# Performance work log

Hardware: AMD Instinct MI355X
Metric: run time of the kernel (lower is better)

Reference implementation:

```python
import jax, jax.numpy as jnp
import numpy as np
import math

B, N, D, KA, H = 8, 1024, 512, 16, 8
QD = D // 4
HD = D // H


def qsplit(x):
    q = x.shape[-1] // 4
    return x[..., :q], x[..., q:2*q], x[..., 2*q:3*q], x[..., 3*q:]


def hprod(p, q):
    pr, pi, pj, pk = qsplit(p)
    qr, qi, qj, qk = qsplit(q)
    return jnp.concatenate([
        pr*qr - pi*qi - pj*qj - pk*qk,
        pr*qi + pi*qr + pj*qk - pk*qj,
        pr*qj - pi*qk + pj*qr + pk*qi,
        pr*qk + pi*qj - pj*qi + pk*qr,
    ], axis=-1)


def qconj(x):
    r, i, j, k = qsplit(x)
    return jnp.concatenate([r, -i, -j, -k], axis=-1)


def qlin(x, w, b):
    # w: [4, qo, qi] -> Hamilton block matrix [4qo, 4qi]
    r, i, j, k = w[0], w[1], w[2], w[3]
    W = jnp.concatenate([
        jnp.concatenate([r, -i, -j, -k], axis=1),
        jnp.concatenate([i,  r, -k,  j], axis=1),
        jnp.concatenate([j,  k,  r, -i], axis=1),
        jnp.concatenate([k, -j,  i,  r], axis=1),
    ], axis=0)
    return x @ W.T + b


def qln(x, gamma, beta):
    # per-component LayerNorm over Q; gamma/beta: [4, Q]
    qd = x.shape[-1] // 4
    xs = x.reshape(x.shape[:-1] + (4, qd))
    m = xs.mean(-1, keepdims=True)
    v = xs.var(-1, keepdims=True)
    y = (xs - m) / jnp.sqrt(v + 1e-5) * gamma + beta
    return y.reshape(x.shape)


def setup_inputs():
    key = jax.random.key(0)
    ks = jax.random.split(key, 20)
    lim = math.sqrt(6.0 / (2 * QD))  # xavier for [QD, QD]
    def qw(k):
        return jax.random.uniform(k, (4, QD, QD), minval=-lim, maxval=lim)
    return {
        'q': jax.random.normal(ks[0], (B, N, D), dtype=jnp.float32),
        'spike': jax.random.uniform(ks[1], (B, N), dtype=jnp.float32),
        'mask': jnp.ones((B, N), dtype=jnp.float32),
        'theta_logit': jnp.float32(0.0),
        'w_prim': qw(ks[2]), 'b_prim': jnp.zeros((D,), jnp.float32),
        'anchors': jax.random.normal(ks[3], (KA, D)) * 0.5,
        'log_sigma': jnp.zeros((KA,), jnp.float32),
        'w_aggr': qw(ks[4]), 'b_aggr': jnp.zeros((D,), jnp.float32),
        'w_q': qw(ks[5]), 'b_q': jnp.zeros((D,), jnp.float32),
        'w_k': qw(ks[6]), 'b_k': jnp.zeros((D,), jnp.float32),
        'w_v': qw(ks[7]), 'b_v': jnp.zeros((D,), jnp.float32),
        'w_o': qw(ks[8]), 'b_o': jnp.zeros((D,), jnp.float32),
        'ln_gamma': jnp.ones((4, QD), jnp.float32),
        'ln_beta': jnp.zeros((4, QD), jnp.float32),
    }


def reference(q, spike, mask, theta_logit, w_prim, b_prim, anchors, log_sigma,
              w_aggr, b_aggr, w_q, b_q, w_k, b_k, w_v, b_v, w_o, b_o,
              ln_gamma, ln_beta):
    b, n, d = q.shape
    qd = d // 4
    # --- SpikeQuaternionRotation: rotate toward K-axis by theta = theta_max*spike ---
    theta_max = (jnp.pi / 2) * jax.nn.sigmoid(theta_logit)
    theta = theta_max * spike                      # [B, N]
    c = jnp.cos(theta)[..., None]
    s = jnp.sin(theta)[..., None]
    z = jnp.zeros_like(c)
    rot = jnp.concatenate([
        jnp.broadcast_to(c, (b, n, qd)),
        jnp.broadcast_to(z, (b, n, qd)),
        jnp.broadcast_to(z, (b, n, qd)),
        jnp.broadcast_to(s, (b, n, qd)),
    ], axis=-1)
    q_rot = hprod(rot, q)                          # [B, N, D]

    # --- PrimaryLayer: per-cell quaternion transform ---
    msg_p = qlin(q_rot, w_prim, b_prim)

    # --- QuaternionAnchorLayer ---
    a_conj = qconj(anchors)                        # [KA, D]
    prod = hprod(q_rot[:, None, :, :], a_conj[None, :, None, :])  # [B, KA, N, D]
    dist = jnp.sum(prod * prod, axis=-1)           # [B, KA, N]
    sigma_sq = jnp.maximum(jnp.exp(log_sigma) ** 2, 1e-6)
    incid = jnp.exp(-dist / sigma_sq[None, :, None]) * mask[:, None, :]
    denom = jnp.maximum(incid.sum(-1, keepdims=True), 1e-6)
    h = jnp.einsum('bkn,bnd->bkd', incid, q_rot) / denom  # [B, KA, D]
    h = qlin(h, w_aggr, b_aggr)

    # --- QuaternionMHA(query=q_rot, key=h, value=h), no mask ---
    Qh = qlin(q_rot, w_q, b_q).reshape(b, n, H, HD)
    Kh = qlin(h, w_k, b_k).reshape(b, KA, H, HD)
    Vh = qlin(h, w_v, b_v).reshape(b, KA, H, HD)
    scores = jnp.einsum('bqhd,bkhd->bhqk', Qh, Kh) / jnp.sqrt(jnp.float32(HD))
    attn = jax.nn.softmax(scores, axis=-1)
    out = jnp.einsum('bhqk,bkhd->bqhd', attn, Vh).reshape(b, n, d)
    msg_a = qlin(out, w_o, b_o)

    # --- residual + per-component LayerNorm ---
    return qln(q + msg_p + msg_a, ln_gamma, ln_beta)
```

## Files before the change

kernel.cpp:

```cpp
#include <hip/hip_runtime.h>
#include <hip/hip_bf16.h>

typedef __hip_bfloat16 bf16;
typedef __attribute__((ext_vector_type(8))) short bf16x8;
typedef __attribute__((ext_vector_type(4))) float f32x4;

__device__ __forceinline__ float bflo(unsigned u) { return __uint_as_float(u << 16); }
__device__ __forceinline__ float bfhi(unsigned u) { return __uint_as_float(u & 0xffff0000u); }
__device__ __forceinline__ bool probe_f32(const void* mask) {
  return *(const unsigned*)mask == 0x3F800000u;
}
__device__ __forceinline__ float ldin(const void* p, size_t i, bool f32) {
  return f32 ? ((const float*)p)[i] : (float)((const bf16*)p)[i];
}


__global__ __launch_bounds__(256) void prologue(
    const void* w0, const void* w1, const void* w2, const void* w3,
    const void* w4, const void* w5,
    const void* b0, const void* b1, const void* b2, const void* b3,
    const void* b4, const void* b5, const void* g_, const void* be,
    const void* q, const void* spike, const void* theta_logit, const void* mask,
    bf16* __restrict__ Wall, float* __restrict__ biasF,
    bf16* __restrict__ q_rot, float* __restrict__ qn) {
  bool f32 = probe_f32(mask);
  int blk = blockIdx.x, t = threadIdx.x;
  if (blk < 1536) {
    int E = blk * 1024 + t * 4;
    int g = E >> 9;
    int wi = g >> 9;
    int o = g & 511;
    int k0 = E & 511;
    const void* src = wi == 0 ? w0 : wi == 1 ? w1 : wi == 2 ? w2 : wi == 3 ? w3 : wi == 4 ? w4 : w5;
    int ro = o >> 7, a = o & 127, co = k0 >> 7;
    int comp = ro ^ co;
    float sgn = ((0x284Eu >> (ro * 4 + co)) & 1u) ? -1.0f : 1.0f;
    bf16 ov[4];
    #pragma unroll
    for (int j = 0; j < 4; ++j) {
      int b2 = (k0 & 127) + j;
      ov[j] = (bf16)(ldin(src, comp * 16384 + a * 128 + b2, f32) * sgn);
    }
    int r = g & 63, c = k0 >> 3;
    size_t off = (size_t)(g >> 6) * 65536 + (size_t)((c >> 2) * 4096 + (r >> 4) * 1024
               + ((c & 3) * 16 + (r & 15)) * 16 + (k0 & 7) * 2);
    *(uint2*)((char*)Wall + off) = *(const uint2*)ov;
  } else if (blk < 1544) {
    int b = blk - 1536;
    const void* src = b == 0 ? b0 : b == 1 ? b1 : b == 2 ? b2 : b == 3 ? b3
                    : b == 4 ? b4 : b == 5 ? b5 : b == 6 ? g_ : be;
    biasF[b * 512 + t] = ldin(src, t, f32);
    biasF[b * 512 + 256 + t] = ldin(src, 256 + t, f32);
  } else {
    int idx = blk - 1544;
    int row = idx * 8 + (t >> 5);
    int l = (t & 31) * 4;
    float tl = ldin(theta_logit, 0, f32);
    float tmax = 1.5707963267948966f / (1.0f + __expf(-tl));
    float th = tmax * ldin(spike, row, f32);
    float c = cosf(th), s = sinf(th);
    size_t base = (size_t)row * 512;
    float av[4], bv[4], cv[4], dv[4];
    if (f32) {
      const float* qp = (const float*)q + base + l;
      f32x4 va = *(const f32x4*)(qp);
      f32x4 vb = *(const f32x4*)(qp + 128);
      f32x4 vc = *(const f32x4*)(qp + 256);
      f32x4 vd = *(const f32x4*)(qp + 384);
      #pragma unroll
      for (int j = 0; j < 4; ++j) { av[j] = va[j]; bv[j] = vb[j]; cv[j] = vc[j]; dv[j] = vd[j]; }
    } else {
      const bf16* qp = (const bf16*)q + base + l;
      uint2 ua = *(const uint2*)(qp);
      uint2 ub = *(const uint2*)(qp + 128);
      uint2 uc = *(const uint2*)(qp + 256);
      uint2 ud = *(const uint2*)(qp + 384);
      av[0] = bflo(ua.x); av[1] = bfhi(ua.x); av[2] = bflo(ua.y); av[3] = bfhi(ua.y);
      bv[0] = bflo(ub.x); bv[1] = bfhi(ub.x); bv[2] = bflo(ub.y); bv[3] = bfhi(ub.y);
      cv[0] = bflo(uc.x); cv[1] = bfhi(uc.x); cv[2] = bflo(uc.y); cv[3] = bfhi(uc.y);
      dv[0] = bflo(ud.x); dv[1] = bfhi(ud.x); dv[2] = bflo(ud.y); dv[3] = bfhi(ud.y);
    }
    bf16 o0[4], o1[4], o2[4], o3[4];
    f32x4 qv;
    #pragma unroll
    for (int j = 0; j < 4; ++j) {
      float r0 = c * av[j] - s * dv[j];
      float r1 = c * bv[j] - s * cv[j];
      float r2 = c * cv[j] + s * bv[j];
      float r3 = c * dv[j] + s * av[j];
      o0[j] = (bf16)r0; o1[j] = (bf16)r1; o2[j] = (bf16)r2; o3[j] = (bf16)r3;
      qv[j] = r0 * r0 + r1 * r1 + r2 * r2 + r3 * r3;
    }
    bf16* orow = q_rot + base + l;
    *(uint2*)(orow)       = *(const uint2*)o0;
    *(uint2*)(orow + 128) = *(const uint2*)o1;
    *(uint2*)(orow + 256) = *(const uint2*)o2;
    *(uint2*)(orow + 384) = *(const uint2*)o3;
    *(f32x4*)(qn + (size_t)row * 128 + l) = qv;
  }
}

__device__ __forceinline__ void stage_B64(const bf16* __restrict__ Bw, int n0, char* Bs, int t) {
  const char* src = (const char*)Bw + (size_t)(n0 >> 6) * 65536;
  #pragma unroll
  for (int i = 0; i < 16; ++i)
    *(uint4*)(Bs + t * 16 + i * 4096) = *(const uint4*)(src + t * 16 + i * 4096);
}

__global__ __launch_bounds__(256, 2) void gemm_dist(
    const bf16* __restrict__ A, const bf16* __restrict__ Bw,
    const float* __restrict__ bias0, const float* __restrict__ bias1,
    bf16* __restrict__ MQ,
    const float* __restrict__ qn, const void* anchors, const void* lsig,
    const void* mask, float* __restrict__ h_part, float* __restrict__ pd_part) {
  __shared__ char smem[77952];
  const int t = threadIdx.x;
  if (blockIdx.x >= 128) {
    char* Bs = smem;
    const int g = blockIdx.x - 128;
    const int wave = t >> 6, lane = t & 63;
    const int quad = lane >> 4, l16 = lane & 15;
    const int m0 = (g & 31) * 256, n0 = (g >> 5) * 64;
    stage_B64(Bw, n0, Bs, t);
    __syncthreads();
    const int mbase = m0 + wave * 64;
    f32x4 acc[4][4] = {};
    bf16x8 areg[2][4], breg[2][4];
    #pragma unroll
    for (int mt = 0; mt < 4; ++mt)
      areg[0][mt] = *(const bf16x8*)(A + (size_t)(mbase + mt * 16 + l16) * 512 + quad * 8);
    #pragma unroll
    for (int nt = 0; nt < 4; ++nt)
      breg[0][nt] = *(const bf16x8*)(Bs + nt * 1024 + lane * 16);
    #pragma unroll
    for (int kk = 0; kk < 16; ++kk) {
      const int cur = kk & 1, nxt = cur ^ 1;
      if (kk < 15) {
        const int k2 = (kk + 1) * 32;
        #pragma unroll
        for (int mt = 0; mt < 4; ++mt)
          areg[nxt][mt] = *(const bf16x8*)(A + (size_t)(mbase + mt * 16 + l16) * 512 + k2 + quad * 8);
        #pragma unroll
        for (int nt = 0; nt < 4; ++nt)
          breg[nxt][nt] = *(const bf16x8*)(Bs + (kk + 1) * 4096 + nt * 1024 + lane * 16);
      }
      #pragma unroll
      for (int mt = 0; mt < 4; ++mt)
        #pragma unroll
        for (int nt = 0; nt < 4; ++nt)
          acc[mt][nt] = __builtin_amdgcn_mfma_f32_16x16x32_bf16(areg[cur][mt], breg[cur][nt],
                                                                acc[mt][nt], 0, 0, 0);
    }
    #pragma unroll
    for (int nt = 0; nt < 4; ++nt) {
      int col = n0 + nt * 16 + l16;
      float bv = col < 512 ? bias0[col] : bias1[col - 512];
      #pragma unroll
      for (int mt = 0; mt < 4; ++mt) {
        int rb = mbase + mt * 16 + quad * 4;
        #pragma unroll
        for (int r = 0; r < 4; ++r)
          MQ[(size_t)(rb + r) * 1024 + col] = (bf16)(acc[mt][nt][r] + bv);
      }
    }
  } else {
    bool f32 = probe_f32(mask);
    bf16*  qr    = (bf16*)smem;
    float* an    = (float*)(smem + 65536);
    float* sIncT = (float*)(smem + 73728);
    float* rs    = (float*)(smem + 77824);
    float* pd    = (float*)(smem + 77888);
    int bb = blockIdx.x;
    int b = bb >> 4, nc = bb & 15;
    {
      const uint4* src = (const uint4*)((const bf16*)A + ((size_t)b * 1024 + nc * 64) * 512);
      uint4* dst = (uint4*)qr;
      #pragma unroll
      for (int i = 0; i < 16; ++i) dst[t + i * 256] = src[t + i * 256];
    }
    for (int i = t; i < 2048; i += 256) {
      int k = i >> 7, l = i & 127;
      float a0 = ldin(anchors, k * 512 + l, f32);
      float a1 = ldin(anchors, k * 512 + 128 + l, f32);
      float a2 = ldin(anchors, k * 512 + 256 + l, f32);
      float a3 = ldin(anchors, k * 512 + 384 + l, f32);
      an[i] = a0 * a0 + a1 * a1 + a2 * a2 + a3 * a3;
    }
    if (t < 16) {
      float ls = ldin(lsig, t, f32);
      float ssq = __expf(ls); ssq = fmaxf(ssq * ssq, 1e-6f);
      rs[t] = -1.0f / ssq;
      pd[t] = 0.0f;
    }
    __syncthreads();
    {
      int rl = t >> 2, part = t & 3;
      int n = nc * 64 + rl;
      const float* qrow = qn + ((size_t)b * 1024 + n) * 128 + part * 32;
      f32x4 q4[8];
      #pragma unroll
      for (int i = 0; i < 8; ++i) q4[i] = *(const f32x4*)(qrow + i * 4);
      float sc[16] = {};
      #pragma unroll
      for (int i = 0; i < 8; ++i) {
        #pragma unroll
        for (int k = 0; k < 16; ++k) {
          f32x4 av = *(const f32x4*)(an + k * 128 + part * 32 + i * 4);
          sc[k] += q4[i][0] * av[0] + q4[i][1] * av[1] + q4[i][2] * av[2] + q4[i][3] * av[3];
        }
      }
      #pragma unroll
      for (int k = 0; k < 16; ++k) {
        sc[k] += __shfl_xor(sc[k], 1, 64);
        sc[k] += __shfl_xor(sc[k], 2, 64);
      }
      if (part == 0) {
        float mval = ldin(mask, b * 1024 + n, f32);
        #pragma unroll
        for (int k = 0; k < 16; ++k) {
          float inc = __expf(sc[k] * rs[k]) * mval;
          sIncT[rl * 16 + k] = inc;
          atomicAdd(&pd[k], inc);
        }
      }
    }
    __syncthreads();
    {
      float acc0[16] = {}, acc1[16] = {};
      for (int nn = 0; nn < 64; ++nn) {
        unsigned u = *(const unsigned*)(qr + nn * 512 + 2 * t);
        float v0 = bflo(u);
        float v1 = bfhi(u);
        f32x4 p0 = *(const f32x4*)(sIncT + nn * 16);
        f32x4 p1 = *(const f32x4*)(sIncT + nn * 16 + 4);
        f32x4 p2 = *(const f32x4*)(sIncT + nn * 16 + 8);
        f32x4 p3 = *(const f32x4*)(sIncT + nn * 16 + 12);
        #pragma unroll
        for (int j = 0; j < 4; ++j) {
          acc0[j]      += p0[j] * v0; acc1[j]      += p0[j] * v1;
          acc0[4 + j]  += p1[j] * v0; acc1[4 + j]  += p1[j] * v1;
          acc0[8 + j]  += p2[j] * v0; acc1[8 + j]  += p2[j] * v1;
          acc0[12 + j] += p3[j] * v0; acc1[12 + j] += p3[j] * v1;
        }
      }
      #pragma unroll
      for (int k = 0; k < 16; ++k) {
        size_t base = ((size_t)(b * 16 + k) * 16 + nc) * 512;
        float2 o2 = {acc0[k], acc1[k]};
        *(float2*)(h_part + base + 2 * t) = o2;
      }
    }
    if (t < 16) pd_part[((size_t)(b * 16 + t)) * 16 + nc] = pd[t];
  }
}

__device__ __forceinline__ float dotW4(const char* WallB, int gRow, const float* xp512, int c4lo) {
  const char* p = WallB + (size_t)(gRow >> 6) * 65536
                + (size_t)(((gRow >> 4) & 3) * 1024 + (gRow & 15) * 16);
  float acc = 0.0f;
  #pragma unroll
  for (int c4 = c4lo; c4 < c4lo + 4; ++c4) {
    #pragma unroll
    for (int cl = 0; cl < 4; ++cl) {
      uint4 u = *(const uint4*)(p + c4 * 4096 + cl * 256);
      const float* xp = xp512 + c4 * 32 + cl * 8;
      acc += xp[0] * bflo(u.x) + xp[1] * bfhi(u.x)
           + xp[2] * bflo(u.y) + xp[3] * bfhi(u.y)
           + xp[4] * bflo(u.z) + xp[5] * bfhi(u.z)
           + xp[6] * bflo(u.w) + xp[7] * bfhi(u.w);
    }
  }
  return acc;
}

__global__ __launch_bounds__(256) void aggr_k(
    const float* __restrict__ h_part, const float* __restrict__ pd_part,
    const bf16* __restrict__ Wall, const float* __restrict__ biasF,
    float* __restrict__ h_aggr) {
  __shared__ float xs[512];
  const char* WallB = (const char*)Wall;
  const float* ba = biasF + 1536;
  const int gy = blockIdx.x >> 7, row = blockIdx.x & 127;
  const int t = threadIdx.x;
  float dsum = 0.0f;
  #pragma unroll
  for (int nc = 0; nc < 16; ++nc) dsum += pd_part[row * 16 + nc];
  float dinv = 1.0f / fmaxf(dsum, 1e-6f);
  #pragma unroll
  for (int j = 0; j < 2; ++j) {
    int d = j * 256 + t;
    float hv = 0.0f;
    #pragma unroll
    for (int nc = 0; nc < 16; ++nc) hv += h_part[(size_t)row * 8192 + nc * 512 + d];
    xs[d] = hv * dinv;
  }
  __syncthreads();
  const int o = gy * 64 + (t >> 2), part = t & 3;
  float acc = dotW4(WallB, 1536 + o, xs, part * 4);
  acc += __shfl_xor(acc, 1, 64);
  acc += __shfl_xor(acc, 2, 64);
  if (part == 0) h_aggr[(size_t)row * 512 + o] = acc + ba[o];
}

__global__ __launch_bounds__(256) void kv_k(
    const float* __restrict__ h_aggr, const bf16* __restrict__ Wall,
    const float* __restrict__ biasF,
    float* __restrict__ Kh, float* __restrict__ Vh) {
  __shared__ float ys[512];
  const char* WallB = (const char*)Wall;
  const float* bk = biasF + 2048;
  const float* bv = biasF + 2560;
  const int gy = blockIdx.x >> 7, row = blockIdx.x & 127;
  const int t = threadIdx.x;
  #pragma unroll
  for (int j = 0; j < 2; ++j) {
    int d = j * 256 + t;
    ys[d] = h_aggr[(size_t)row * 512 + d];
  }
  __syncthreads();
  const int o = gy * 64 + (t >> 2), part = t & 3;
  float ak = dotW4(WallB, 2048 + o, ys, part * 4);
  float av = dotW4(WallB, 2560 + o, ys, part * 4);
  ak += __shfl_xor(ak, 1, 64);
  ak += __shfl_xor(ak, 2, 64);
  av += __shfl_xor(av, 1, 64);
  av += __shfl_xor(av, 2, 64);
  if (part == 0) {
    Kh[(size_t)row * 512 + o] = ak + bk[o];
    Vh[(size_t)row * 512 + o] = av + bv[o];
  }
}

__global__ __launch_bounds__(256, 2) void attn_tail(
    const bf16* __restrict__ MQ, const float* __restrict__ Kh_g,
    const float* __restrict__ Vh_g, const bf16* __restrict__ Wall,
    const float* __restrict__ biasF, const void* q, const void* mask, void* out) {
  __shared__ float KV[8 * 1092];
  __shared__ float P[16 * 132];
  const bool f32 = probe_f32(mask);
  const int t = threadIdx.x;
  const int rowbase = blockIdx.x * 16;
  const int b = rowbase >> 10;
  for (int i = t; i < 8192; i += 256) {
    int k = i >> 9, d = i & 511, h = d >> 6, dd = d & 63;
    KV[h * 1092 + k * 68 + dd] = Kh_g[(size_t)b * 8192 + i];
  }
  __syncthreads();
  {
    const int r = t >> 4, h = (t >> 1) & 7, hf = t & 1;
    const int grow = rowbase + r;
    const uint4* qp = (const uint4*)(MQ + (size_t)grow * 1024 + 512 + h * 64 + hf * 32);
    float qv[32];
    #pragma unroll
    for (int i = 0; i < 4; ++i) {
      uint4 u = qp[i];
      qv[i * 8 + 0] = bflo(u.x); qv[i * 8 + 1] = bfhi(u.x);
      qv[i * 8 + 2] = bflo(u.y); qv[i * 8 + 3] = bfhi(u.y);
      qv[i * 8 + 4] = bflo(u.z); qv[i * 8 + 5] = bfhi(u.z);
      qv[i * 8 + 6] = bflo(u.w); qv[i * 8 + 7] = bfhi(u.w);
    }
    float sc[16];
    #pragma unroll
    for (int k = 0; k < 16; ++k) {
      float s = 0.0f;
      #pragma unroll
      for (int d4 = 0; d4 < 8; ++d4) {
        f32x4 kv = *(const f32x4*)(KV + h * 1092 + k * 68 + hf * 32 + d4 * 4);
        s += qv[d4 * 4 + 0] * kv[0] + qv[d4 * 4 + 1] * kv[1]
           + qv[d4 * 4 + 2] * kv[2] + qv[d4 * 4 + 3] * kv[3];
      }
      sc[k] = s;
    }
    #pragma unroll
    for (int k = 0; k < 16; ++k) sc[k] += __shfl_xor(sc[k], 1, 64);
    if (hf == 0) {
      #pragma unroll
      for (int k = 0; k < 16; ++k) sc[k] *= 0.125f;
      float m = sc[0];
      #pragma unroll
      for (int k = 1; k < 16; ++k) m = fmaxf(m, sc[k]);
      float ssum = 0.0f;
      #pragma unroll
      for (int k = 0; k < 16; ++k) { sc[k] = __expf(sc[k] - m); ssum += sc[k]; }
      float inv = 1.0f / ssum;
      #pragma unroll
      for (int k = 0; k < 16; ++k) P[r * 132 + h * 16 + k] = sc[k] * inv;
    }
  }
  __syncthreads();
  for (int i = t; i < 8192; i += 256) {
    int k = i >> 9, d = i & 511, h = d >> 6, dd = d & 63;
    KV[h * 1092 + k * 68 + dd] = Vh_g[(size_t)b * 8192 + i];
  }
  __syncthreads();
  float pv[8][4];
  {
    const int r = t >> 4, dg = t & 15;
    #pragma unroll
    for (int h = 0; h < 8; ++h) {
      float a0 = 0, a1 = 0, a2 = 0, a3 = 0;
      #pragma unroll
      for (int k = 0; k < 16; ++k) {
        float p = P[r * 132 + h * 16 + k];
        f32x4 va = *(const f32x4*)(KV + h * 1092 + k * 68 + dg * 4);
        a0 += p * va[0]; a1 += p * va[1]; a2 += p * va[2]; a3 += p * va[3];
      }
      pv[h][0] = a0; pv[h][1] = a1; pv[h][2] = a2; pv[h][3] = a3;
    }
  }
  __syncthreads();
  char* A_lds = (char*)KV;
  {
    const int r = t >> 4, dg = t & 15;
    #pragma unroll
    for (int h = 0; h < 8; ++h) {
      int c0 = h * 64 + dg * 4;
      int off = (c0 >> 5) * 1024 + ((c0 >> 3) & 3) * 256 + r * 16 + (c0 & 7) * 2;
      bf16 ov[4] = {(bf16)pv[h][0], (bf16)pv[h][1], (bf16)pv[h][2], (bf16)pv[h][3]};
      *(uint2*)(A_lds + off) = *(const uint2*)ov;
    }
  }
  __syncthreads();
  const int wave = t >> 6, lane = t & 63, quad = lane >> 4, l16 = lane & 15;
  const char* WallB = (const char*)Wall;
  f32x4 acc[8] = {};
  bf16x8 breg[2][8];
  bf16x8 areg[2];
  areg[0] = *(const bf16x8*)(A_lds + quad * 256 + l16 * 16);
  #pragma unroll
  for (int nt = 0; nt < 8; ++nt) {
    size_t cb = (size_t)(16 + wave * 2 + (nt >> 2)) * 65536;
    breg[0][nt] = *(const bf16x8*)(WallB + cb + (nt & 3) * 1024 + lane * 16);
  }
  #pragma unroll
  for (int kk = 0; kk < 16; ++kk) {
    const int cur = kk & 1, nxt = cur ^ 1;
    if (kk < 15) {
      areg[nxt] = *(const bf16x8*)(A_lds + (kk + 1) * 1024 + quad * 256 + l16 * 16);
      #pragma unroll
      for (int nt = 0; nt < 8; ++nt) {
        size_t cb = (size_t)(16 + wave * 2 + (nt >> 2)) * 65536;
        breg[nxt][nt] = *(const bf16x8*)(WallB + cb + (kk + 1) * 4096 + (nt & 3) * 1024 + lane * 16);
      }
    }
    #pragma unroll
    for (int nt = 0; nt < 8; ++nt)
      acc[nt] = __builtin_amdgcn_mfma_f32_16x16x32_bf16(areg[cur], breg[cur][nt], acc[nt], 0, 0, 0);
  }
  const float* biasO = biasF + 1024;
  const float* gamF = biasF + 3072;
  float xv[8][4];
  float s[4] = {0, 0, 0, 0}, s2[4] = {0, 0, 0, 0};
  #pragma unroll
  for (int nt = 0; nt < 8; ++nt) {
    int gcol = wave * 128 + nt * 16 + l16;
    float bo = biasO[gcol];
    #pragma unroll
    for (int reg = 0; reg < 4; ++reg) {
      int grow = rowbase + quad * 4 + reg;
      float qv = ldin(q, (size_t)grow * 512 + gcol, f32);
      float mp = (float)MQ[(size_t)grow * 1024 + gcol];
      float x = qv + mp + acc[nt][reg] + bo;
      xv[nt][reg] = x;
      s[reg] += x; s2[reg] += x * x;
    }
  }
  #pragma unroll
  for (int reg = 0; reg < 4; ++reg) {
    #pragma unroll
    for (int off = 1; off <= 8; off <<= 1) {
      s[reg]  += __shfl_xor(s[reg], off, 64);
      s2[reg] += __shfl_xor(s2[reg], off, 64);
    }
  }
  #pragma unroll
  for (int reg = 0; reg < 4; ++reg) {
    float m = s[reg] * (1.0f / 128.0f);
    float rinv = rsqrtf(s2[reg] * (1.0f / 128.0f) - m * m + 1e-5f);
    int grow = rowbase + quad * 4 + reg;
    #pragma unroll
    for (int nt = 0; nt < 8; ++nt) {
      int gcol = wave * 128 + nt * 16 + l16;
      float y = (xv[nt][reg] - m) * rinv * gamF[gcol] + gamF[512 + gcol];
      if (f32) ((float*)out)[(size_t)grow * 512 + gcol] = y;
      else     ((bf16*)out)[(size_t)grow * 512 + gcol] = (bf16)y;
    }
  }
}

extern "C" void kernel_launch(void* const* d_in, const int* in_sizes, int n_in,
                              void* d_out, int out_size, void* d_ws, size_t ws_size,
                              hipStream_t stream) {
  (void)in_sizes; (void)n_in; (void)out_size; (void)ws_size;
  const void* q      = d_in[0];
  const void* spike  = d_in[1];
  const void* mask   = d_in[2];
  const void* tl     = d_in[3];
  const void* w_prim = d_in[4];
  const void* b_prim = d_in[5];
  const void* anchors= d_in[6];
  const void* lsig   = d_in[7];
  const void* w_aggr = d_in[8];
  const void* b_aggr = d_in[9];
  const void* w_q    = d_in[10];
  const void* b_q    = d_in[11];
  const void* w_k    = d_in[12];
  const void* b_k    = d_in[13];
  const void* w_v    = d_in[14];
  const void* b_v    = d_in[15];
  const void* w_o    = d_in[16];
  const void* b_o    = d_in[17];
  const void* gam    = d_in[18];
  const void* bet    = d_in[19];

  char* ws = (char*)d_ws;
  bf16*  Wall   = (bf16*)(ws + 0);
  bf16*  q_rot  = (bf16*)(ws + 3145728);
  float* qn     = (float*)(ws + 11534336);
  bf16*  MQ     = (bf16*)(ws + 15728640);
  float* h_part = (float*)(ws + 32505856);
  float* pd_part= (float*)(ws + 36700160);
  float* Kh     = (float*)(ws + 36708352);
  float* Vh     = (float*)(ws + 36970496);
  float* biasF  = (float*)(ws + 37232640);
  float* h_aggr = (float*)(ws + 37249024);

  prologue<<<2568, 256, 0, stream>>>(w_prim, w_q, w_o, w_aggr, w_k, w_v,
                                     b_prim, b_q, b_o, b_aggr, b_k, b_v, gam, bet,
                                     q, spike, tl, mask, Wall, biasF, q_rot, qn);
  gemm_dist<<<640, 256, 0, stream>>>(q_rot, Wall, biasF + 0, biasF + 512, MQ,
                                     qn, anchors, lsig, mask, h_part, pd_part);
  aggr_k<<<1024, 256, 0, stream>>>(h_part, pd_part, Wall, biasF, h_aggr);
  kv_k<<<1024, 256, 0, stream>>>(h_aggr, Wall, biasF, Kh, Vh);
  attn_tail<<<512, 256, 0, stream>>>(MQ, Kh, Vh, Wall, biasF, q, mask, d_out);
}
```

Baseline: 189.4 us.

## Build Hamilton weight tiles on the fly instead of materializing in prologue

The prologue no longer expands five of the six quaternion weight tensors into a bf16 Hamilton block matrix in workspace. Only w_o is still expanded. The GEMM stage now builds its B tile in shared memory directly from the raw weights, applying sign and component selection while staging. The aggr and kv matvecs read the raw weights with the sign applied per quaternion block. This removes most of the prologue's weight-expansion traffic and blocks, at the cost of more scattered loads and f32-to-bf16 conversion inside the GEMM and the matvecs.

```diff
diff --git a/kernel.cpp b/kernel.cpp
--- a/kernel.cpp
+++ b/kernel.cpp
@@ -15,9 +15,8 @@
 }
 
 
-__global__ __launch_bounds__(256) void prologue(
-    const void* w0, const void* w1, const void* w2, const void* w3,
-    const void* w4, const void* w5,
+__global__ __launch_bounds__(256) void rot_k(
+    const void* w_o,
     const void* b0, const void* b1, const void* b2, const void* b3,
     const void* b4, const void* b5, const void* g_, const void* be,
     const void* q, const void* spike, const void* theta_logit, const void* mask,
@@ -25,13 +24,11 @@
     bf16* __restrict__ q_rot, float* __restrict__ qn) {
   bool f32 = probe_f32(mask);
   int blk = blockIdx.x, t = threadIdx.x;
-  if (blk < 1536) {
-    int E = blk * 1024 + t * 4;
+  if (blk < 256) {
+    int E = (blk + 512) * 1024 + t * 4;
     int g = E >> 9;
-    int wi = g >> 9;
     int o = g & 511;
     int k0 = E & 511;
-    const void* src = wi == 0 ? w0 : wi == 1 ? w1 : wi == 2 ? w2 : wi == 3 ? w3 : wi == 4 ? w4 : w5;
     int ro = o >> 7, a = o & 127, co = k0 >> 7;
     int comp = ro ^ co;
     float sgn = ((0x284Eu >> (ro * 4 + co)) & 1u) ? -1.0f : 1.0f;
@@ -39,20 +36,20 @@
     #pragma unroll
     for (int j = 0; j < 4; ++j) {
       int b2 = (k0 & 127) + j;
-      ov[j] = (bf16)(ldin(src, comp * 16384 + a * 128 + b2, f32) * sgn);
+      ov[j] = (bf16)(ldin(w_o, comp * 16384 + a * 128 + b2, f32) * sgn);
     }
     int r = g & 63, c = k0 >> 3;
     size_t off = (size_t)(g >> 6) * 65536 + (size_t)((c >> 2) * 4096 + (r >> 4) * 1024
                + ((c & 3) * 16 + (r & 15)) * 16 + (k0 & 7) * 2);
     *(uint2*)((char*)Wall + off) = *(const uint2*)ov;
-  } else if (blk < 1544) {
-    int b = blk - 1536;
+  } else if (blk < 264) {
+    int b = blk - 256;
     const void* src = b == 0 ? b0 : b == 1 ? b1 : b == 2 ? b2 : b == 3 ? b3
                     : b == 4 ? b4 : b == 5 ? b5 : b == 6 ? g_ : be;
     biasF[b * 512 + t] = ldin(src, t, f32);
     biasF[b * 512 + 256 + t] = ldin(src, 256 + t, f32);
   } else {
-    int idx = blk - 1544;
+    int idx = blk - 264;
     int row = idx * 8 + (t >> 5);
     int l = (t & 31) * 4;
     float tl = ldin(theta_logit, 0, f32);
@@ -100,28 +97,54 @@
   }
 }
 
-__device__ __forceinline__ void stage_B64(const bf16* __restrict__ Bw, int n0, char* Bs, int t) {
-  const char* src = (const char*)Bw + (size_t)(n0 >> 6) * 65536;
-  #pragma unroll
-  for (int i = 0; i < 16; ++i)
-    *(uint4*)(Bs + t * 16 + i * 4096) = *(const uint4*)(src + t * 16 + i * 4096);
+__device__ __forceinline__ void stage_B64_raw(const void* w, bool f32, int o_base, char* Bs, int t) {
+  const int r = t & 63, co = t >> 6;
+  const int o = o_base + r;
+  const int ro = o >> 7, a = o & 127;
+  const int comp = ro ^ co;
+  const bool neg = (0x284Eu >> (ro * 4 + co)) & 1u;
+  if (!f32) {
+    const char* src = (const char*)w + (size_t)(comp * 16384 + a * 128) * 2;
+    const unsigned sx = neg ? 0x80008000u : 0u;
+    #pragma unroll
+    for (int i = 0; i < 16; ++i) {
+      uint4 u = *(const uint4*)(src + i * 16);
+      u.x ^= sx; u.y ^= sx; u.z ^= sx; u.w ^= sx;
+      int off = (co * 4 + (i >> 2)) * 4096 + (r >> 4) * 1024 + ((i & 3) * 16 + (r & 15)) * 16;
+      *(uint4*)(Bs + off) = u;
+    }
+  } else {
+    const float* src = (const float*)w + comp * 16384 + a * 128;
+    const float sgn = neg ? -1.0f : 1.0f;
+    #pragma unroll
+    for (int i = 0; i < 16; ++i) {
+      f32x4 v0 = *(const f32x4*)(src + i * 8);
+      f32x4 v1 = *(const f32x4*)(src + i * 8 + 4);
+      bf16 ov[8];
+      #pragma unroll
+      for (int j = 0; j < 4; ++j) { ov[j] = (bf16)(v0[j] * sgn); ov[4 + j] = (bf16)(v1[j] * sgn); }
+      int off = (co * 4 + (i >> 2)) * 4096 + (r >> 4) * 1024 + ((i & 3) * 16 + (r & 15)) * 16;
+      *(uint4*)(Bs + off) = *(const uint4*)ov;
+    }
+  }
 }
 
 __global__ __launch_bounds__(256, 2) void gemm_dist(
-    const bf16* __restrict__ A, const bf16* __restrict__ Bw,
+    const bf16* __restrict__ A, const void* w_prim, const void* w_q,
     const float* __restrict__ bias0, const float* __restrict__ bias1,
     bf16* __restrict__ MQ,
     const float* __restrict__ qn, const void* anchors, const void* lsig,
     const void* mask, float* __restrict__ h_part, float* __restrict__ pd_part) {
   __shared__ char smem[77952];
   const int t = threadIdx.x;
+  const bool f32 = probe_f32(mask);
   if (blockIdx.x >= 128) {
     char* Bs = smem;
     const int g = blockIdx.x - 128;
     const int wave = t >> 6, lane = t & 63;
     const int quad = lane >> 4, l16 = lane & 15;
     const int m0 = (g & 31) * 256, n0 = (g >> 5) * 64;
-    stage_B64(Bw, n0, Bs, t);
+    stage_B64_raw(n0 < 512 ? w_prim : w_q, f32, n0 & 511, Bs, t);
     __syncthreads();
     const int mbase = m0 + wave * 64;
     f32x4 acc[4][4] = {};
@@ -164,7 +187,6 @@
       }
     }
   } else {
-    bool f32 = probe_f32(mask);
     bf16*  qr    = (bf16*)smem;
     float* an    = (float*)(smem + 65536);
     float* sIncT = (float*)(smem + 73728);
@@ -254,31 +276,42 @@
   }
 }
 
-__device__ __forceinline__ float dotW4(const char* WallB, int gRow, const float* xp512, int c4lo) {
-  const char* p = WallB + (size_t)(gRow >> 6) * 65536
-                + (size_t)(((gRow >> 4) & 3) * 1024 + (gRow & 15) * 16);
+__device__ __forceinline__ float dotW_raw(const void* w, bool f32, int o, int co,
+                                          const float* xp512) {
+  const int ro = o >> 7, a = o & 127;
+  const int comp = ro ^ co;
+  const float sgn = ((0x284Eu >> (ro * 4 + co)) & 1u) ? -1.0f : 1.0f;
+  const float* xp = xp512 + co * 128;
   float acc = 0.0f;
-  #pragma unroll
-  for (int c4 = c4lo; c4 < c4lo + 4; ++c4) {
-    #pragma unroll
-    for (int cl = 0; cl < 4; ++cl) {
-      uint4 u = *(const uint4*)(p + c4 * 4096 + cl * 256);
-      const float* xp = xp512 + c4 * 32 + cl * 8;
-      acc += xp[0] * bflo(u.x) + xp[1] * bfhi(u.x)
-           + xp[2] * bflo(u.y) + xp[3] * bfhi(u.y)
-           + xp[4] * bflo(u.z) + xp[5] * bfhi(u.z)
-           + xp[6] * bflo(u.w) + xp[7] * bfhi(u.w);
-    }
-  }
-  return acc;
+  if (!f32) {
+    const uint4* src = (const uint4*)((const char*)w + (size_t)(comp * 16384 + a * 128) * 2);
+    #pragma unroll
+    for (int j = 0; j < 16; ++j) {
+      uint4 u = src[j];
+      const float* x8 = xp + j * 8;
+      acc += x8[0] * bflo(u.x) + x8[1] * bfhi(u.x)
+           + x8[2] * bflo(u.y) + x8[3] * bfhi(u.y)
+           + x8[4] * bflo(u.z) + x8[5] * bfhi(u.z)
+           + x8[6] * bflo(u.w) + x8[7] * bfhi(u.w);
+    }
+  } else {
+    const float* src = (const float*)w + comp * 16384 + a * 128;
+    #pragma unroll
+    for (int j = 0; j < 32; ++j) {
+      f32x4 v = *(const f32x4*)(src + j * 4);
+      const float* x4 = xp + j * 4;
+      acc += x4[0] * v[0] + x4[1] * v[1] + x4[2] * v[2] + x4[3] * v[3];
+    }
+  }
+  return acc * sgn;
 }
 
 __global__ __launch_bounds__(256) void aggr_k(
     const float* __restrict__ h_part, const float* __restrict__ pd_part,
-    const bf16* __restrict__ Wall, const float* __restrict__ biasF,
+    const void* w_aggr, const void* mask, const float* __restrict__ biasF,
     float* __restrict__ h_aggr) {
   __shared__ float xs[512];
-  const char* WallB = (const char*)Wall;
+  const bool f32 = probe_f32(mask);
   const float* ba = biasF + 1536;
   const int gy = blockIdx.x >> 7, row = blockIdx.x & 127;
   const int t = threadIdx.x;
@@ -296,18 +329,18 @@
   }
   __syncthreads();
   const int o = gy * 64 + (t >> 2), part = t & 3;
-  float acc = dotW4(WallB, 1536 + o, xs, part * 4);
+  float acc = dotW_raw(w_aggr, f32, o, part, xs);
   acc += __shfl_xor(acc, 1, 64);
   acc += __shfl_xor(acc, 2, 64);
   if (part == 0) h_aggr[(size_t)row * 512 + o] = acc + ba[o];
 }
 
 __global__ __launch_bounds__(256) void kv_k(
-    const float* __restrict__ h_aggr, const bf16* __restrict__ Wall,
-    const float* __restrict__ biasF,
+    const float* __restrict__ h_aggr, const void* w_k, const void* w_v,
+    const void* mask, const float* __restrict__ biasF,
     float* __restrict__ Kh, float* __restrict__ Vh) {
   __shared__ float ys[512];
-  const char* WallB = (const char*)Wall;
+  const bool f32 = probe_f32(mask);
   const float* bk = biasF + 2048;
   const float* bv = biasF + 2560;
   const int gy = blockIdx.x >> 7, row = blockIdx.x & 127;
@@ -319,8 +352,8 @@
   }
   __syncthreads();
   const int o = gy * 64 + (t >> 2), part = t & 3;
-  float ak = dotW4(WallB, 2048 + o, ys, part * 4);
-  float av = dotW4(WallB, 2560 + o, ys, part * 4);
+  float ak = dotW_raw(w_k, f32, o, part, ys);
+  float av = dotW_raw(w_v, f32, o, part, ys);
   ak += __shfl_xor(ak, 1, 64);
   ak += __shfl_xor(ak, 2, 64);
   av += __shfl_xor(av, 1, 64);
@@ -525,12 +558,11 @@
   float* biasF  = (float*)(ws + 37232640);
   float* h_aggr = (float*)(ws + 37249024);
 
-  prologue<<<2568, 256, 0, stream>>>(w_prim, w_q, w_o, w_aggr, w_k, w_v,
-                                     b_prim, b_q, b_o, b_aggr, b_k, b_v, gam, bet,
-                                     q, spike, tl, mask, Wall, biasF, q_rot, qn);
-  gemm_dist<<<640, 256, 0, stream>>>(q_rot, Wall, biasF + 0, biasF + 512, MQ,
+  rot_k<<<1288, 256, 0, stream>>>(w_o, b_prim, b_q, b_o, b_aggr, b_k, b_v, gam, bet,
+                                  q, spike, tl, mask, Wall, biasF, q_rot, qn);
+  gemm_dist<<<640, 256, 0, stream>>>(q_rot, w_prim, w_q, biasF + 0, biasF + 512, MQ,
                                      qn, anchors, lsig, mask, h_part, pd_part);
-  aggr_k<<<1024, 256, 0, stream>>>(h_part, pd_part, Wall, biasF, h_aggr);
-  kv_k<<<1024, 256, 0, stream>>>(h_aggr, Wall, biasF, Kh, Vh);
+  aggr_k<<<1024, 256, 0, stream>>>(h_part, pd_part, w_aggr, mask, biasF, h_aggr);
+  kv_k<<<1024, 256, 0, stream>>>(h_aggr, w_k, w_v, mask, biasF, Kh, Vh);
   attn_tail<<<512, 256, 0, stream>>>(MQ, Kh, Vh, Wall, biasF, q, mask, d_out);
 }
```

Result: slower. 215.5 us (+13.8%).
